# Optimization experiments

Measured on AMD Instinct MI355X. Metric: run time of the kernel, lower is better.

Reference implementation:

```python
import jax, jax.numpy as jnp
import numpy as np

LX, LY = 16, 16
N = 2 * LX * LY        # 512 lattice sites (sequence length)
NH = 128               # GRU hidden size
K = 2                  # binary occupation categories
NS = 4096              # number of Monte-Carlo samples (batch)


def setup_inputs() -> dict:
    key = jax.random.key(0)
    k0, k1, k2, k3 = jax.random.split(key, 4)
    gru_kernel = jax.random.normal(k0, (K, 3 * NH), jnp.float32) * (1.0 / np.sqrt(K))
    gru_rkernel = jax.random.normal(k1, (NH, 3 * NH), jnp.float32) * (1.0 / np.sqrt(NH))
    gru_bias = jnp.zeros((2, 3 * NH), jnp.float32)  # [input_bias; recurrent_bias] (reset_after=True)
    dense_w = jax.random.normal(k2, (NH, K), jnp.float32) * (1.0 / np.sqrt(NH))
    dense_b = jnp.zeros((K,), jnp.float32)
    u = jax.random.uniform(k3, (NS, N), jnp.float32)  # pre-drawn noise for categorical draws
    return {"gru_kernel": gru_kernel, "gru_rkernel": gru_rkernel, "gru_bias": gru_bias,
            "dense_w": dense_w, "dense_b": dense_b, "u": u}


def reference(gru_kernel, gru_rkernel, gru_bias, dense_w, dense_b, u):
    """Autoregressive GRU sampling over N lattice sites.
    Returns (samples [ns,N] int32, log_prob [ns] float32)."""
    ns = u.shape[0]
    b_in, b_rec = gru_bias[0], gru_bias[1]

    def step(carry, u_t):
        h, x = carry                       # h: [ns,NH], x: one-hot prev sample [ns,K]
        xg = x @ gru_kernel + b_in          # [ns,3NH]
        hg = h @ gru_rkernel + b_rec        # [ns,3NH]
        xz, xr, xh = jnp.split(xg, 3, axis=-1)   # keras gate order: z, r, h
        hz, hr, hh = jnp.split(hg, 3, axis=-1)
        z = jax.nn.sigmoid(xz + hz)
        r = jax.nn.sigmoid(xr + hr)
        hc = jnp.tanh(xh + r * hh)          # reset_after=True candidate
        h_new = z * h + (1.0 - z) * hc
        probs = jax.nn.softmax(h_new @ dense_w + dense_b, axis=-1)  # [ns,K]
        p1 = probs[:, 1]
        s = (u_t < p1).astype(jnp.int32)    # categorical draw (K=2) via inverse CDF
        logp_t = jnp.log(jnp.where(s == 1, p1, probs[:, 0]) + 1e-10)
        x_new = jax.nn.one_hot(s, K, dtype=h.dtype)
        return (h_new, x_new), (s, logp_t)

    h0 = jnp.zeros((ns, NH), u.dtype)
    x0 = jnp.zeros((ns, K), u.dtype)        # zero input at first site
    (_, _), (samples, logps) = jax.lax.scan(step, (h0, x0), u.T)  # scan over N sites
    return samples.T, logps.sum(axis=0)
```

## Files before the change

kernel.cpp:

```cpp
#include <hip/hip_runtime.h>

#define NHID   128
#define NSTEPS 512
#define NSAMP  4096
#define SPB    16
#define BS     512
#define NBLK   (NSAMP / SPB)
#define SAMP_ELEMS (NSAMP * NSTEPS)
#define WT_ELEMS   (3 * NHID * NHID)

__global__ __launch_bounds__(256)
void pack_w_kernel(const float* __restrict__ rk, float* __restrict__ wt) {
    const int i = blockIdx.x * 256 + threadIdx.x;
    if (i < WT_ELEMS) {
        const int j  = i & 3;
        const int c  = (i >> 2) & 127;
        const int k4 = (i >> 9) & 31;
        const int g  = i >> 14;
        wt[i] = rk[(k4 * 4 + j) * 384 + g * NHID + c];
    }
}

template<int TR>
__global__ __launch_bounds__(BS, 1)
void vmc_gru_kernel(const float* __restrict__ gk,
                    const float* __restrict__ rk,
                    const float* __restrict__ gb,
                    const float* __restrict__ dw,
                    const float* __restrict__ db,
                    const float* __restrict__ u,
                    const float* __restrict__ wt,
                    float* __restrict__ out)
{
    __shared__ float hsm[2][NHID][SPB];
    __shared__ float part[2][8][SPB][2];
    __shared__ float uld[NSTEPS][SPB];

    const int tid = threadIdx.x;
    const int cg  = tid >> 2;
    const int sq  = tid & 3;
    const int s0  = sq * 4;
    const int wv  = tid >> 6;

    {
        const int sl = tid >> 5;
        const int t0 = (tid & 31) * 16;
        const float* up = u + (size_t)(blockIdx.x * SPB + sl) * NSTEPS + t0;
        const float4 a = ((const float4*)up)[0];
        const float4 b = ((const float4*)up)[1];
        const float4 c = ((const float4*)up)[2];
        const float4 d = ((const float4*)up)[3];
        const float tmp[16] = {a.x,a.y,a.z,a.w, b.x,b.y,b.z,b.w,
                               c.x,c.y,c.z,c.w, d.x,d.y,d.z,d.w};
        #pragma unroll
        for (int i = 0; i < 16; ++i) uld[t0 + i][sl] = tmp[i];
    }
    for (int i = tid; i < NHID * SPB; i += BS) (&hsm[0][0][0])[i] = 0.0f;
    __syncthreads();

    const float brz = gb[384 + cg];
    const float brr = gb[384 + 128 + cg];
    const float brh = gb[384 + 256 + cg];
    const float xzI = gb[cg],       xz0c = xzI + gk[cg],       xz1c = xzI + gk[384 + cg];
    const float xrI = gb[128 + cg], xr0c = xrI + gk[128 + cg], xr1c = xrI + gk[384 + 128 + cg];
    const float xhI = gb[256 + cg], xh0c = xhI + gk[256 + cg], xh1c = xhI + gk[384 + 256 + cg];
    const float dwc0 = dw[cg * 2], dwc1 = dw[cg * 2 + 1];
    const float db0 = db[0], db1 = db[1];

    const float4* wz4 = (const float4*)wt + cg;
    const float4* wr4 = (const float4*)wt + 4096 + cg;
    const float4* wh4 = (const float4*)wt + 8192 + cg;
    const float* rkp = rk + cg;

    int   pv[4] = {0, 0, 0, 0};
    float lg[4] = {0.f, 0.f, 0.f, 0.f};
    int cur = 0;

    for (int t = 0; t < NSTEPS; ++t) {
        float az[4] = {brz, brz, brz, brz};
        float ar[4] = {brr, brr, brr, brr};
        float ah[4] = {brh, brh, brh, brh};

        if (TR) {
            #pragma unroll 4
            for (int k4 = 0; k4 < 32; ++k4) {
                const float4 wz = wz4[k4 * 128];
                const float4 wr = wr4[k4 * 128];
                const float4 wh = wh4[k4 * 128];
                const float4 h0 = *(const float4*)&hsm[cur][4 * k4 + 0][s0];
                const float4 h1 = *(const float4*)&hsm[cur][4 * k4 + 1][s0];
                const float4 h2 = *(const float4*)&hsm[cur][4 * k4 + 2][s0];
                const float4 h3 = *(const float4*)&hsm[cur][4 * k4 + 3][s0];
                const float hk0[4] = {h0.x, h0.y, h0.z, h0.w};
                const float hk1[4] = {h1.x, h1.y, h1.z, h1.w};
                const float hk2[4] = {h2.x, h2.y, h2.z, h2.w};
                const float hk3[4] = {h3.x, h3.y, h3.z, h3.w};
                #pragma unroll
                for (int j = 0; j < 4; ++j) az[j] = fmaf(wz.x, hk0[j], az[j]);
                #pragma unroll
                for (int j = 0; j < 4; ++j) ar[j] = fmaf(wr.x, hk0[j], ar[j]);
                #pragma unroll
                for (int j = 0; j < 4; ++j) ah[j] = fmaf(wh.x, hk0[j], ah[j]);
                #pragma unroll
                for (int j = 0; j < 4; ++j) az[j] = fmaf(wz.y, hk1[j], az[j]);
                #pragma unroll
                for (int j = 0; j < 4; ++j) ar[j] = fmaf(wr.y, hk1[j], ar[j]);
                #pragma unroll
                for (int j = 0; j < 4; ++j) ah[j] = fmaf(wh.y, hk1[j], ah[j]);
                #pragma unroll
                for (int j = 0; j < 4; ++j) az[j] = fmaf(wz.z, hk2[j], az[j]);
                #pragma unroll
                for (int j = 0; j < 4; ++j) ar[j] = fmaf(wr.z, hk2[j], ar[j]);
                #pragma unroll
                for (int j = 0; j < 4; ++j) ah[j] = fmaf(wh.z, hk2[j], ah[j]);
                #pragma unroll
                for (int j = 0; j < 4; ++j) az[j] = fmaf(wz.w, hk3[j], az[j]);
                #pragma unroll
                for (int j = 0; j < 4; ++j) ar[j] = fmaf(wr.w, hk3[j], ar[j]);
                #pragma unroll
                for (int j = 0; j < 4; ++j) ah[j] = fmaf(wh.w, hk3[j], ah[j]);
            }
        } else {
            const float* wp = rkp;
            #pragma unroll 4
            for (int k = 0; k < NHID; ++k) {
                const float wz = wp[0];
                const float wr = wp[NHID];
                const float wh = wp[2 * NHID];
                const float4 hv = *(const float4*)&hsm[cur][k][s0];
                const float hk[4] = {hv.x, hv.y, hv.z, hv.w};
                #pragma unroll
                for (int j = 0; j < 4; ++j) az[j] = fmaf(wz, hk[j], az[j]);
                #pragma unroll
                for (int j = 0; j < 4; ++j) ar[j] = fmaf(wr, hk[j], ar[j]);
                #pragma unroll
                for (int j = 0; j < 4; ++j) ah[j] = fmaf(wh, hk[j], ah[j]);
                wp += 3 * NHID;
            }
        }

        const float4 ho = *(const float4*)&hsm[cur][cg][s0];
        const float hov[4] = {ho.x, ho.y, ho.z, ho.w};
        float hn[4], p0s[4], p1s[4];
        #pragma unroll
        for (int j = 0; j < 4; ++j) {
            float xz = pv[j] ? xz1c : xz0c;
            float xr = pv[j] ? xr1c : xr0c;
            float xh = pv[j] ? xh1c : xh0c;
            if (t == 0) { xz = xzI; xr = xrI; xh = xhI; }
            const float z  = 1.0f / (1.0f + expf(-(xz + az[j])));
            const float r  = 1.0f / (1.0f + expf(-(xr + ar[j])));
            const float hc = tanhf(xh + r * ah[j]);
            const float hnew = z * hov[j] + (1.0f - z) * hc;
            hn[j] = hnew;
            p0s[j] = hnew * dwc0;
            p1s[j] = hnew * dwc1;
        }
        *(float4*)&hsm[cur ^ 1][cg][s0] = make_float4(hn[0], hn[1], hn[2], hn[3]);

        #pragma unroll
        for (int off = 4; off < 64; off <<= 1) {
            #pragma unroll
            for (int j = 0; j < 4; ++j) {
                p0s[j] += __shfl_xor(p0s[j], off);
                p1s[j] += __shfl_xor(p1s[j], off);
            }
        }
        const int pb = t & 1;
        if ((tid & 63) < 4) {
            *(float4*)&part[pb][wv][s0][0]     = make_float4(p0s[0], p1s[0], p0s[1], p1s[1]);
            *(float4*)&part[pb][wv][s0 + 2][0] = make_float4(p0s[2], p1s[2], p0s[3], p1s[3]);
        }
        __syncthreads();

        float l0[4] = {db0, db0, db0, db0};
        float l1[4] = {db1, db1, db1, db1};
        #pragma unroll
        for (int w = 0; w < 8; ++w) {
            const float4 qa = *(const float4*)&part[pb][w][s0][0];
            const float4 qb = *(const float4*)&part[pb][w][s0 + 2][0];
            l0[0] += qa.x; l1[0] += qa.y;
            l0[1] += qa.z; l1[1] += qa.w;
            l0[2] += qb.x; l1[2] += qb.y;
            l0[3] += qb.z; l1[3] += qb.w;
        }
        const float4 uu = *(const float4*)&uld[t][s0];
        const float uv[4] = {uu.x, uu.y, uu.z, uu.w};
        #pragma unroll
        for (int j = 0; j < 4; ++j) {
            const float mx = fmaxf(l0[j], l1[j]);
            const float e0 = expf(l0[j] - mx);
            const float e1 = expf(l1[j] - mx);
            const float inv = 1.0f / (e0 + e1);
            const float p1v = e1 * inv;
            const int st = (uv[j] < p1v) ? 1 : 0;
            const float psel = st ? p1v : (e0 * inv);
            lg[j] += logf(psel + 1e-10f);
            pv[j] = st;
            if (cg == 0)
                out[(size_t)(blockIdx.x * SPB + s0 + j) * NSTEPS + t] = (float)st;
        }
        cur ^= 1;
    }

    if (cg == 0) {
        #pragma unroll
        for (int j = 0; j < 4; ++j)
            out[SAMP_ELEMS + blockIdx.x * SPB + s0 + j] = lg[j];
    }
}

extern "C" void kernel_launch(void* const* d_in, const int* in_sizes, int n_in,
                              void* d_out, int out_size, void* d_ws, size_t ws_size,
                              hipStream_t stream) {
    const float* gk = (const float*)d_in[0];
    const float* rk = (const float*)d_in[1];
    const float* gb = (const float*)d_in[2];
    const float* dw = (const float*)d_in[3];
    const float* db = (const float*)d_in[4];
    const float* u  = (const float*)d_in[5];
    float* out = (float*)d_out;

    if (ws_size >= (size_t)WT_ELEMS * sizeof(float)) {
        float* wt = (float*)d_ws;
        pack_w_kernel<<<(WT_ELEMS + 255) / 256, 256, 0, stream>>>(rk, wt);
        vmc_gru_kernel<1><<<NBLK, BS, 0, stream>>>(gk, rk, gb, dw, db, u, wt, out);
    } else {
        vmc_gru_kernel<0><<<NBLK, BS, 0, stream>>>(gk, rk, gb, dw, db, u, rk, out);
    }
}
```

Measured before the change: 4.440 ms.

## Stage part of recurrent weights in LDS and use packed FMA2

Copies the first 17 of 32 k4-slices of each gate's packed recurrent weights into shared memory once per block, so the per-step GEMV reads that part from LDS instead of global/L2. The remaining slices still stream from global memory. The FMAs are also rewritten with 2-wide vector types, so the compiler can emit packed v_pk_fma_f32 instructions. The cost is about 104KB of extra LDS, which holds occupancy at one block per CU, and more LDS bandwidth pressure alongside the h-state reads.

```diff
diff --git a/kernel.cpp b/kernel.cpp
--- a/kernel.cpp
+++ b/kernel.cpp
@@ -6,8 +6,24 @@
 #define SPB    16
 #define BS     512
 #define NBLK   (NSAMP / SPB)
+#define KL4    17
 #define SAMP_ELEMS (NSAMP * NSTEPS)
 #define WT_ELEMS   (3 * NHID * NHID)
+
+typedef float v2f __attribute__((ext_vector_type(2)));
+typedef float v4f __attribute__((ext_vector_type(4)));
+
+static __device__ __forceinline__ v2f fma2(v2f a, v2f b, v2f c) {
+#if defined(__has_builtin)
+#if __has_builtin(__builtin_elementwise_fma)
+    return __builtin_elementwise_fma(a, b, c);
+#else
+    return (v2f){fmaf(a.x, b.x, c.x), fmaf(a.y, b.y, c.y)};
+#endif
+#else
+    return (v2f){fmaf(a.x, b.x, c.x), fmaf(a.y, b.y, c.y)};
+#endif
+}
 
 __global__ __launch_bounds__(256)
 void pack_w_kernel(const float* __restrict__ rk, float* __restrict__ wt) {
@@ -32,9 +48,10 @@
                     const float* __restrict__ wt,
                     float* __restrict__ out)
 {
-    __shared__ float hsm[2][NHID][SPB];
-    __shared__ float part[2][8][SPB][2];
-    __shared__ float uld[NSTEPS][SPB];
+    __shared__ float  hsm[2][NHID][SPB];
+    __shared__ float  part[2][8][SPB][2];
+    __shared__ float  uld[NSTEPS][SPB];
+    __shared__ float4 slds[3 * KL4 * NHID];
 
     const int tid = threadIdx.x;
     const int cg  = tid >> 2;
@@ -55,6 +72,14 @@
         #pragma unroll
         for (int i = 0; i < 16; ++i) uld[t0 + i][sl] = tmp[i];
     }
+    if (TR) {
+        const float4* wt4 = (const float4*)wt;
+        for (int i = tid; i < 3 * KL4 * NHID; i += BS) {
+            const int g  = i / (KL4 * NHID);
+            const int r  = i - g * (KL4 * NHID);
+            slds[i] = wt4[g * 4096 + r];
+        }
+    }
     for (int i = tid; i < NHID * SPB; i += BS) (&hsm[0][0][0])[i] = 0.0f;
     __syncthreads();
 
@@ -67,9 +92,12 @@
     const float dwc0 = dw[cg * 2], dwc1 = dw[cg * 2 + 1];
     const float db0 = db[0], db1 = db[1];
 
-    const float4* wz4 = (const float4*)wt + cg;
-    const float4* wr4 = (const float4*)wt + 4096 + cg;
-    const float4* wh4 = (const float4*)wt + 8192 + cg;
+    const v4f* lz = (const v4f*)slds + cg;
+    const v4f* lr = (const v4f*)slds + KL4 * 128 + cg;
+    const v4f* lh = (const v4f*)slds + 2 * KL4 * 128 + cg;
+    const v4f* wz4 = (const v4f*)wt + cg;
+    const v4f* wr4 = (const v4f*)wt + 4096 + cg;
+    const v4f* wh4 = (const v4f*)wt + 8192 + cg;
     const float* rkp = rk + cg;
 
     int   pv[4] = {0, 0, 0, 0};
@@ -77,48 +105,42 @@
     int cur = 0;
 
     for (int t = 0; t < NSTEPS; ++t) {
-        float az[4] = {brz, brz, brz, brz};
-        float ar[4] = {brr, brr, brr, brr};
-        float ah[4] = {brh, brh, brh, brh};
+        v2f az01 = {brz, brz}, az23 = {brz, brz};
+        v2f ar01 = {brr, brr}, ar23 = {brr, brr};
+        v2f ah01 = {brh, brh}, ah23 = {brh, brh};
+
+#define GEMM_K4(WZ, WR, WH, K4) do {                                        \
+    const v4f h_0 = *(const v4f*)&hsm[cur][4*(K4)+0][s0];                   \
+    const v4f h_1 = *(const v4f*)&hsm[cur][4*(K4)+1][s0];                   \
+    const v4f h_2 = *(const v4f*)&hsm[cur][4*(K4)+2][s0];                   \
+    const v4f hh[4] = {h_0, h_1, h_2, *(const v4f*)&hsm[cur][4*(K4)+3][s0]};\
+    _Pragma("unroll")                                                        \
+    for (int kk = 0; kk < 4; ++kk) {                                         \
+        const v2f hlo = hh[kk].xy;                                           \
+        const v2f hhi = hh[kk].zw;                                           \
+        const v2f wz2 = {(WZ)[kk], (WZ)[kk]};                                \
+        const v2f wr2 = {(WR)[kk], (WR)[kk]};                                \
+        const v2f wh2 = {(WH)[kk], (WH)[kk]};                                \
+        az01 = fma2(wz2, hlo, az01); az23 = fma2(wz2, hhi, az23);            \
+        ar01 = fma2(wr2, hlo, ar01); ar23 = fma2(wr2, hhi, ar23);            \
+        ah01 = fma2(wh2, hlo, ah01); ah23 = fma2(wh2, hhi, ah23);            \
+    }                                                                         \
+} while (0)
 
         if (TR) {
             #pragma unroll 4
-            for (int k4 = 0; k4 < 32; ++k4) {
-                const float4 wz = wz4[k4 * 128];
-                const float4 wr = wr4[k4 * 128];
-                const float4 wh = wh4[k4 * 128];
-                const float4 h0 = *(const float4*)&hsm[cur][4 * k4 + 0][s0];
-                const float4 h1 = *(const float4*)&hsm[cur][4 * k4 + 1][s0];
-                const float4 h2 = *(const float4*)&hsm[cur][4 * k4 + 2][s0];
-                const float4 h3 = *(const float4*)&hsm[cur][4 * k4 + 3][s0];
-                const float hk0[4] = {h0.x, h0.y, h0.z, h0.w};
-                const float hk1[4] = {h1.x, h1.y, h1.z, h1.w};
-                const float hk2[4] = {h2.x, h2.y, h2.z, h2.w};
-                const float hk3[4] = {h3.x, h3.y, h3.z, h3.w};
-                #pragma unroll
-                for (int j = 0; j < 4; ++j) az[j] = fmaf(wz.x, hk0[j], az[j]);
-                #pragma unroll
-                for (int j = 0; j < 4; ++j) ar[j] = fmaf(wr.x, hk0[j], ar[j]);
-                #pragma unroll
-                for (int j = 0; j < 4; ++j) ah[j] = fmaf(wh.x, hk0[j], ah[j]);
-                #pragma unroll
-                for (int j = 0; j < 4; ++j) az[j] = fmaf(wz.y, hk1[j], az[j]);
-                #pragma unroll
-                for (int j = 0; j < 4; ++j) ar[j] = fmaf(wr.y, hk1[j], ar[j]);
-                #pragma unroll
-                for (int j = 0; j < 4; ++j) ah[j] = fmaf(wh.y, hk1[j], ah[j]);
-                #pragma unroll
-                for (int j = 0; j < 4; ++j) az[j] = fmaf(wz.z, hk2[j], az[j]);
-                #pragma unroll
-                for (int j = 0; j < 4; ++j) ar[j] = fmaf(wr.z, hk2[j], ar[j]);
-                #pragma unroll
-                for (int j = 0; j < 4; ++j) ah[j] = fmaf(wh.z, hk2[j], ah[j]);
-                #pragma unroll
-                for (int j = 0; j < 4; ++j) az[j] = fmaf(wz.w, hk3[j], az[j]);
-                #pragma unroll
-                for (int j = 0; j < 4; ++j) ar[j] = fmaf(wr.w, hk3[j], ar[j]);
-                #pragma unroll
-                for (int j = 0; j < 4; ++j) ah[j] = fmaf(wh.w, hk3[j], ah[j]);
+            for (int k4 = 0; k4 < KL4; ++k4) {
+                const v4f wz = lz[k4 * 128];
+                const v4f wr = lr[k4 * 128];
+                const v4f wh = lh[k4 * 128];
+                GEMM_K4(wz, wr, wh, k4);
+            }
+            #pragma unroll 4
+            for (int k4 = KL4; k4 < 32; ++k4) {
+                const v4f wz = wz4[k4 * 128];
+                const v4f wr = wr4[k4 * 128];
+                const v4f wh = wh4[k4 * 128];
+                GEMM_K4(wz, wr, wh, k4);
             }
         } else {
             const float* wp = rkp;
@@ -127,19 +149,22 @@
                 const float wz = wp[0];
                 const float wr = wp[NHID];
                 const float wh = wp[2 * NHID];
-                const float4 hv = *(const float4*)&hsm[cur][k][s0];
-                const float hk[4] = {hv.x, hv.y, hv.z, hv.w};
-                #pragma unroll
-                for (int j = 0; j < 4; ++j) az[j] = fmaf(wz, hk[j], az[j]);
-                #pragma unroll
-                for (int j = 0; j < 4; ++j) ar[j] = fmaf(wr, hk[j], ar[j]);
-                #pragma unroll
-                for (int j = 0; j < 4; ++j) ah[j] = fmaf(wh, hk[j], ah[j]);
+                const v4f hv = *(const v4f*)&hsm[cur][k][s0];
+                const v2f hlo = hv.xy, hhi = hv.zw;
+                const v2f wz2 = {wz, wz}, wr2 = {wr, wr}, wh2 = {wh, wh};
+                az01 = fma2(wz2, hlo, az01); az23 = fma2(wz2, hhi, az23);
+                ar01 = fma2(wr2, hlo, ar01); ar23 = fma2(wr2, hhi, ar23);
+                ah01 = fma2(wh2, hlo, ah01); ah23 = fma2(wh2, hhi, ah23);
                 wp += 3 * NHID;
             }
         }
-
-        const float4 ho = *(const float4*)&hsm[cur][cg][s0];
+#undef GEMM_K4
+
+        const float az[4] = {az01.x, az01.y, az23.x, az23.y};
+        const float ar[4] = {ar01.x, ar01.y, ar23.x, ar23.y};
+        const float ah[4] = {ah01.x, ah01.y, ah23.x, ah23.y};
+
+        const v4f ho = *(const v4f*)&hsm[cur][cg][s0];
         const float hov[4] = {ho.x, ho.y, ho.z, ho.w};
         float hn[4], p0s[4], p1s[4];
         #pragma unroll
@@ -156,7 +181,7 @@
             p0s[j] = hnew * dwc0;
             p1s[j] = hnew * dwc1;
         }
-        *(float4*)&hsm[cur ^ 1][cg][s0] = make_float4(hn[0], hn[1], hn[2], hn[3]);
+        *(v4f*)&hsm[cur ^ 1][cg][s0] = (v4f){hn[0], hn[1], hn[2], hn[3]};
 
         #pragma unroll
         for (int off = 4; off < 64; off <<= 1) {
```

After: 4.228 ms. 4.8% less time.
